# Kernel optimization log

Hardware: AMD Instinct MI355X
Metric: run time of the kernel (lower is better)

The kernel has to match this reference:

```python
import jax, jax.numpy as jnp
import numpy as np

L = 4          # encoder layers
D = 1280       # d_model
H = 20         # heads
DH = D // H
FF = 5120
MEL = 128
S = 1500       # post-conv seq len
EPS = 1e-6


def quant_per_token(x):
    # dynamic per-token int8 quant: scale = max|x|/127
    s = jnp.max(jnp.abs(x), axis=-1, keepdims=True) / 127.0
    s = jnp.maximum(s, 1e-8)
    q = jnp.clip(jnp.round(x / s), -128, 127)
    return q, s


def w8a8_linear(qx, sx, w, b):
    # per-output-channel int8 weight quant, W8A8 GEMM, fp dequant epilogue
    ws = jnp.maximum(jnp.max(jnp.abs(w), axis=1, keepdims=True) / 127.0, 1e-8)  # [O,1]
    qw = jnp.clip(jnp.round(w / ws), -128, 127)
    y = qx @ qw.T                        # int-valued accum in fp32
    return y * sx * ws[:, 0][None, :] + b[None, :]


def rmsnorm_quant(x, w, b):
    # rms_norm_general: w * x / sqrt(E[x^2]+eps) + b, then per-token quant
    inv = jax.lax.rsqrt(jnp.mean(x * x, axis=-1, keepdims=True) + EPS)
    return quant_per_token(x * inv * w[None, :] + b[None, :])


def conv1d(x, w, b, stride, pad):
    y = jax.lax.conv_general_dilated(x, w, (stride,), [(pad, pad)],
                                     dimension_numbers=('NCW', 'OIW', 'NCW'))
    return y + b[None, :, None]


def setup_inputs() -> dict:
    key = jax.random.key(0)
    ks = jax.random.split(key, 24)
    n = lambda k, sh, sc=0.02: jax.random.normal(k, sh, jnp.float32) * sc
    return {
        'input_features': jax.random.normal(ks[0], (1, MEL, 2 * S), jnp.float32),
        'conv1_w': n(ks[1], (D, MEL, 3)), 'conv1_b': n(ks[2], (D,)),
        'conv2_w': n(ks[3], (D, D, 3)), 'conv2_b': n(ks[4], (D,)),
        'pos_emb': n(ks[5], (S, D)),
        'ln1_w': jnp.ones((L, D)), 'ln1_b': n(ks[6], (L, D)),
        'qkv_w': n(ks[7], (L, 3 * D, D)), 'qkv_b': n(ks[8], (L, 3 * D)),
        'out_w': n(ks[9], (L, D, D)), 'out_b': n(ks[10], (L, D)),
        'ln2_w': jnp.ones((L, D)), 'ln2_b': n(ks[11], (L, D)),
        'fc1_w': n(ks[12], (L, FF, D)), 'fc1_b': n(ks[13], (L, FF)),
        'fc2_w': n(ks[14], (L, D, FF)), 'fc2_b': n(ks[15], (L, D)),
        'lnf_w': jnp.ones((D,)), 'lnf_b': n(ks[16], (D,)),
    }


def reference(input_features, conv1_w, conv1_b, conv2_w, conv2_b, pos_emb,
              ln1_w, ln1_b, qkv_w, qkv_b, out_w, out_b,
              ln2_w, ln2_b, fc1_w, fc1_b, fc2_w, fc2_b, lnf_w, lnf_b):
    B = input_features.shape[0]
    h = jax.nn.gelu(conv1d(input_features, conv1_w, conv1_b, 1, 1))
    h = jax.nn.gelu(conv1d(h, conv2_w, conv2_b, 2, 1))
    h = h.transpose(0, 2, 1) + pos_emb[None]          # [B,S,D]
    h = h.reshape(B * S, D)
    scale = DH ** -0.5
    for l in range(L):
        res = h
        qx, sx = rmsnorm_quant(h, ln1_w[l], ln1_b[l])
        qkv = w8a8_linear(qx, sx, qkv_w[l], qkv_b[l])  # [B*S, 3D]
        q, k, v = jnp.split(qkv.reshape(B, S, 3, H, DH), 3, axis=2)
        q, k, v = q[:, :, 0], k[:, :, 0], v[:, :, 0]   # [B,S,H,DH]
        scores = jnp.einsum('bqhd,bkhd->bhqk', q, k) * scale
        attn = jax.nn.softmax(scores, axis=-1)
        ao = jnp.einsum('bhqk,bkhd->bqhd', attn, v).reshape(B * S, D)
        qa, sa = quant_per_token(ao)
        h = res + w8a8_linear(qa, sa, out_w[l], out_b[l])
        res = h
        qx, sx = rmsnorm_quant(h, ln2_w[l], ln2_b[l])
        f1 = w8a8_linear(qx, sx, fc1_w[l], fc1_b[l])
        qm, sm = quant_per_token(jax.nn.gelu(f1))
        h = res + w8a8_linear(qm, sm, fc2_w[l], fc2_b[l])
    h = h.reshape(B, S, D)
    # avg_pooler: AvgPool1d(kernel=2, stride=2) over time
    h = h.reshape(B, S // 2, 2, D).mean(axis=2)
    # final LayerNorm (true layernorm, fp path)
    mu = jnp.mean(h, axis=-1, keepdims=True)
    var = jnp.mean(jnp.square(h - mu), axis=-1, keepdims=True)
    h = (h - mu) * jax.lax.rsqrt(var + 1e-5) * lnf_w + lnf_b
    return h
```

## Files before the change

### kernel.cpp

```cpp
#include <hip/hip_runtime.h>
#include <stdint.h>

#define S_LEN 1500
#define D_MODEL 1280
#define N_HEAD 20
#define D_HEAD 64
#define FF_DIM 5120
#define N_LAYER 4

typedef int v4i __attribute__((ext_vector_type(4)));


__device__ inline float gelu_tanh(float x) {
    float x3 = x * x * x;
    return 0.5f * x * (1.0f + tanhf(0.7978845608028654f * (x + 0.044715f * x3)));
}

__device__ inline float wred_sum(float v) {
    for (int o = 32; o > 0; o >>= 1) v += __shfl_down(v, o, 64);
    return v;
}
__device__ inline float wred_max(float v) {
    for (int o = 32; o > 0; o >>= 1) v = fmaxf(v, __shfl_down(v, o, 64));
    return v;
}
__device__ inline float block_sum(float v, float* sm4) {
    v = wred_sum(v);
    int w = threadIdx.x >> 6;
    if ((threadIdx.x & 63) == 0) sm4[w] = v;
    __syncthreads();
    float r = sm4[0] + sm4[1] + sm4[2] + sm4[3];
    __syncthreads();
    return r;
}
__device__ inline float block_max(float v, float* sm4) {
    v = wred_max(v);
    int w = threadIdx.x >> 6;
    if ((threadIdx.x & 63) == 0) sm4[w] = v;
    __syncthreads();
    float r = fmaxf(fmaxf(sm4[0], sm4[1]), fmaxf(sm4[2], sm4[3]));
    __syncthreads();
    return r;
}


__global__ __launch_bounds__(256) void im2col1_kernel(
    const float* __restrict__ x, float* __restrict__ A1)
{
    int t = blockIdx.x * 256 + threadIdx.x;
    int col = blockIdx.y;
    if (t >= 3000) return;
    int tap = col >> 7, i = col & 127;
    int src = t - 1 + tap;
    float v = (src >= 0 && src < 3000) ? x[(size_t)i * 3000 + src] : 0.0f;
    A1[(size_t)t * 384 + col] = v;
}

__global__ __launch_bounds__(256) void im2col2_kernel(
    const float* __restrict__ g1, float* __restrict__ A2)
{
    int col = blockIdx.x * 256 + threadIdx.x;
    int t = blockIdx.y;
    if (col >= 3840) return;
    int tap = col / 1280, o = col - tap * 1280;
    int src = 2 * t - 1 + tap;
    float v = (src >= 0 && src < 3000) ? g1[(size_t)src * 1280 + o] : 0.0f;
    A2[(size_t)t * 3840 + col] = v;
}

__global__ __launch_bounds__(256) void wreorder_kernel(
    const float* __restrict__ w, float* __restrict__ wo, int C)
{
    int o = blockIdx.x;
    int KC = 3 * C;
    const float* wr = w + (size_t)o * KC;
    float* orow = wo + (size_t)o * KC;
    for (int col = threadIdx.x; col < KC; col += 256) {
        int tap = col / C, i = col - tap * C;
        orow[col] = wr[i * 3 + tap];
    }
}

template <int EPI>
__global__ __launch_bounds__(256) void gemm_f32_kernel(
    const float* __restrict__ A, const float* __restrict__ W,
    const float* __restrict__ bias, const float* __restrict__ pos,
    float* __restrict__ out, int M, int N, int K)
{
    __shared__ float As[16][68];
    __shared__ float Bs[16][68];
    int tid = threadIdx.x;
    int tx = tid & 15, ty = tid >> 4;
    int m0 = blockIdx.y * 64, n0 = blockIdx.x * 64;
    int lr = tid >> 2;
    int lk = (tid & 3) * 4;
    int am = m0 + lr; if (am >= M) am = M - 1;
    const float* Ap = A + (size_t)am * K + lk;
    const float* Wp = W + (size_t)(n0 + lr) * K + lk;
    float c[4][4] = {};
    for (int k0 = 0; k0 < K; k0 += 16) {
        float4 av = *(const float4*)(Ap + k0);
        float4 wv = *(const float4*)(Wp + k0);
        __syncthreads();
        As[lk + 0][lr] = av.x; As[lk + 1][lr] = av.y; As[lk + 2][lr] = av.z; As[lk + 3][lr] = av.w;
        Bs[lk + 0][lr] = wv.x; Bs[lk + 1][lr] = wv.y; Bs[lk + 2][lr] = wv.z; Bs[lk + 3][lr] = wv.w;
        __syncthreads();
        #pragma unroll
        for (int kk = 0; kk < 16; kk++) {
            float4 a4 = *(const float4*)&As[kk][ty * 4];
            float4 b4 = *(const float4*)&Bs[kk][tx * 4];
            float ar[4] = {a4.x, a4.y, a4.z, a4.w};
            float br[4] = {b4.x, b4.y, b4.z, b4.w};
            #pragma unroll
            for (int i = 0; i < 4; i++)
                #pragma unroll
                for (int j = 0; j < 4; j++)
                    c[i][j] += ar[i] * br[j];
        }
    }
    #pragma unroll
    for (int i = 0; i < 4; i++) {
        int m = m0 + ty * 4 + i;
        if (m >= M) continue;
        #pragma unroll
        for (int j = 0; j < 4; j++) {
            int n = n0 + tx * 4 + j;
            float v = gelu_tanh(c[i][j] + bias[n]);
            if (EPI == 1) v += pos[(size_t)m * N + n];
            out[(size_t)m * N + n] = v;
        }
    }
}


__global__ __launch_bounds__(256) void wquant_kernel(
    const float* __restrict__ w, int8_t* __restrict__ qw,
    float* __restrict__ ws, int K)
{
    int r = blockIdx.x;
    int tid = threadIdx.x;
    __shared__ float sm4[4];
    const float4* wr = (const float4*)(w + (size_t)r * K);
    int n4 = K >> 2;
    float mx = 0.0f;
    for (int i = tid; i < n4; i += 256) {
        float4 v = wr[i];
        mx = fmaxf(mx, fmaxf(fmaxf(fabsf(v.x), fabsf(v.y)), fmaxf(fabsf(v.z), fabsf(v.w))));
    }
    mx = block_max(mx, sm4);
    float sc = fmaxf(mx / 127.0f, 1e-8f);
    if (tid == 0) ws[r] = sc;
    float rs = 1.0f / sc;
    char4* qr = (char4*)(qw + (size_t)r * K);
    for (int i = tid; i < n4; i += 256) {
        float4 v = wr[i];
        char4 q;
        q.x = (int8_t)fminf(fmaxf(rintf(v.x * rs), -128.0f), 127.0f);
        q.y = (int8_t)fminf(fmaxf(rintf(v.y * rs), -128.0f), 127.0f);
        q.z = (int8_t)fminf(fmaxf(rintf(v.z * rs), -128.0f), 127.0f);
        q.w = (int8_t)fminf(fmaxf(rintf(v.w * rs), -128.0f), 127.0f);
        qr[i] = q;
    }
}

__global__ __launch_bounds__(256) void rmsnorm_quant_kernel(
    const float* __restrict__ x, const float* __restrict__ w,
    const float* __restrict__ b, int8_t* __restrict__ q,
    float* __restrict__ sx)
{
    int s = blockIdx.x;
    int tid = threadIdx.x;
    __shared__ float sm4[4];
    const float* xr = x + (size_t)s * D_MODEL;
    float v[5];
    float ss = 0.0f;
    for (int i = 0; i < 5; i++) {
        float t = xr[tid + 256 * i];
        v[i] = t;
        ss += t * t;
    }
    ss = block_sum(ss, sm4);
    float inv = rsqrtf(ss * (1.0f / 1280.0f) + 1e-6f);
    float mx = 0.0f;
    for (int i = 0; i < 5; i++) {
        int idx = tid + 256 * i;
        float t = v[i] * inv * w[idx] + b[idx];
        v[i] = t;
        mx = fmaxf(mx, fabsf(t));
    }
    mx = block_max(mx, sm4);
    float sc = fmaxf(mx / 127.0f, 1e-8f);
    if (tid == 0) sx[s] = sc;
    float rs = 1.0f / sc;
    for (int i = 0; i < 5; i++) {
        float qv = rintf(v[i] * rs);
        qv = fminf(fmaxf(qv, -128.0f), 127.0f);
        q[(size_t)s * D_MODEL + tid + 256 * i] = (int8_t)qv;
    }
}

template <bool GELU>
__global__ __launch_bounds__(256) void quant_kernel(
    const float* __restrict__ x, int8_t* __restrict__ q,
    float* __restrict__ sx, int Dm)
{
    int s = blockIdx.x;
    int tid = threadIdx.x;
    __shared__ float sm4[4];
    const float4* xr = (const float4*)(x + (size_t)s * Dm);
    int n4 = Dm >> 2;
    float mx = 0.0f;
    for (int i = tid; i < n4; i += 256) {
        float4 t = xr[i];
        if (GELU) { t.x = gelu_tanh(t.x); t.y = gelu_tanh(t.y); t.z = gelu_tanh(t.z); t.w = gelu_tanh(t.w); }
        mx = fmaxf(mx, fmaxf(fmaxf(fabsf(t.x), fabsf(t.y)), fmaxf(fabsf(t.z), fabsf(t.w))));
    }
    mx = block_max(mx, sm4);
    float sc = fmaxf(mx / 127.0f, 1e-8f);
    if (tid == 0) sx[s] = sc;
    float rs = 1.0f / sc;
    char4* qr = (char4*)(q + (size_t)s * Dm);
    for (int i = tid; i < n4; i += 256) {
        float4 t = xr[i];
        if (GELU) { t.x = gelu_tanh(t.x); t.y = gelu_tanh(t.y); t.z = gelu_tanh(t.z); t.w = gelu_tanh(t.w); }
        char4 qq;
        qq.x = (int8_t)fminf(fmaxf(rintf(t.x * rs), -128.0f), 127.0f);
        qq.y = (int8_t)fminf(fmaxf(rintf(t.y * rs), -128.0f), 127.0f);
        qq.z = (int8_t)fminf(fmaxf(rintf(t.z * rs), -128.0f), 127.0f);
        qq.w = (int8_t)fminf(fmaxf(rintf(t.w * rs), -128.0f), 127.0f);
        qr[i] = qq;
    }
}

__global__ __launch_bounds__(256) void gemm_w8a8_mfma(
    const int8_t* __restrict__ qx, const float* __restrict__ sx,
    const int8_t* __restrict__ qw, const float* __restrict__ ws,
    const float* __restrict__ bias, const float* __restrict__ res,
    float* __restrict__ out, int M, int O, int K)
{
    int lane = threadIdx.x & 63;
    int wv = threadIdx.x >> 6;
    int l15 = lane & 15;
    int quad = lane >> 4;
    int m_base = blockIdx.y * 64 + wv * 16;
    int n_base = blockIdx.x * 64;

    int ar = m_base + l15; if (ar >= M) ar = M - 1;
    const int8_t* ap = qx + (size_t)ar * K + quad * 16;
    const int8_t* bp = qw + (size_t)(n_base + l15) * K + quad * 16;
    size_t rowK16 = (size_t)16 * K;

    v4i acc0 = {0, 0, 0, 0}, acc1 = {0, 0, 0, 0}, acc2 = {0, 0, 0, 0}, acc3 = {0, 0, 0, 0};
    int nsteps = K >> 6;
    for (int s = 0; s < nsteps; s++) {
        v4i a  = *(const v4i*)(ap + s * 64);
        v4i b0 = *(const v4i*)(bp + s * 64);
        v4i b1 = *(const v4i*)(bp + rowK16 + s * 64);
        v4i b2 = *(const v4i*)(bp + 2 * rowK16 + s * 64);
        v4i b3 = *(const v4i*)(bp + 3 * rowK16 + s * 64);
        acc0 = __builtin_amdgcn_mfma_i32_16x16x64_i8(a, b0, acc0, 0, 0, 0);
        acc1 = __builtin_amdgcn_mfma_i32_16x16x64_i8(a, b1, acc1, 0, 0, 0);
        acc2 = __builtin_amdgcn_mfma_i32_16x16x64_i8(a, b2, acc2, 0, 0, 0);
        acc3 = __builtin_amdgcn_mfma_i32_16x16x64_i8(a, b3, acc3, 0, 0, 0);
    }

    float sxv[4];
    #pragma unroll
    for (int r = 0; r < 4; r++) {
        int m = m_base + quad * 4 + r;
        sxv[r] = (m < M) ? sx[m] : 0.0f;
    }
    v4i accs[4] = {acc0, acc1, acc2, acc3};
    #pragma unroll
    for (int nb = 0; nb < 4; nb++) {
        int n = n_base + nb * 16 + l15;
        float wn = ws[n];
        float bn = bias[n];
        #pragma unroll
        for (int r = 0; r < 4; r++) {
            int m = m_base + quad * 4 + r;
            if (m < M) {
                float y = (float)accs[nb][r] * sxv[r] * wn + bn;
                if (res) y += res[(size_t)m * O + n];
                out[(size_t)m * O + n] = y;
            }
        }
    }
}

__global__ __launch_bounds__(256) void attn_tiled_kernel(
    const float* __restrict__ qkv, float* __restrict__ ao)
{
    __shared__ float Qs[64][68];
    __shared__ float KV[64][68];
    __shared__ float Ps[64][68];
    int h = blockIdx.y;
    int q_tile = blockIdx.x;
    int tid = threadIdx.x;
    int tx = tid & 15, ty = tid >> 4;
    int q0 = ty * 4;
    int d0 = tx * 4;

    {
        int r = tid >> 2;
        int dq = (tid & 3) * 16;
        int qg = q_tile * 64 + r;
        int qc = qg < S_LEN ? qg : S_LEN - 1;
        const float4* src = (const float4*)(qkv + (size_t)qc * 3840 + h * 64 + dq);
        #pragma unroll
        for (int i = 0; i < 4; i++)
            *(float4*)&Qs[r][dq + i * 4] = src[i];
    }

    float O[4][4] = {};
    float m_run[4], l_run[4];
    #pragma unroll
    for (int i = 0; i < 4; i++) { m_run[i] = -INFINITY; l_run[i] = 0.0f; }

    for (int kt = 0; kt < 24; kt++) {
        int kbase = kt * 64;
        int krem = S_LEN - kbase;

        __syncthreads();
        {
            int kk = tid >> 2;
            int dq = (tid & 3) * 16;
            int kg = kbase + kk;
            int kc = kg < S_LEN ? kg : S_LEN - 1;
            const float4* src = (const float4*)(qkv + (size_t)kc * 3840 + 1280 + h * 64 + dq);
            #pragma unroll
            for (int i = 0; i < 4; i++) {
                float4 v = src[i];
                KV[dq + i * 4 + 0][kk] = v.x;
                KV[dq + i * 4 + 1][kk] = v.y;
                KV[dq + i * 4 + 2][kk] = v.z;
                KV[dq + i * 4 + 3][kk] = v.w;
            }
        }
        __syncthreads();

        float s[4][4] = {};
        int k0loc = tx * 4;
        for (int d = 0; d < 64; d += 4) {
            float4 qv[4], kv[4];
            #pragma unroll
            for (int i = 0; i < 4; i++) qv[i] = *(const float4*)&Qs[q0 + i][d];
            #pragma unroll
            for (int dd = 0; dd < 4; dd++) kv[dd] = *(const float4*)&KV[d + dd][k0loc];
            #pragma unroll
            for (int i = 0; i < 4; i++) {
                float qa[4] = {qv[i].x, qv[i].y, qv[i].z, qv[i].w};
                #pragma unroll
                for (int dd = 0; dd < 4; dd++) {
                    float kb[4] = {kv[dd].x, kv[dd].y, kv[dd].z, kv[dd].w};
                    #pragma unroll
                    for (int j = 0; j < 4; j++)
                        s[i][j] += qa[dd] * kb[j];
                }
            }
        }

        #pragma unroll
        for (int i = 0; i < 4; i++)
            #pragma unroll
            for (int j = 0; j < 4; j++) {
                s[i][j] *= 0.125f;
                if (k0loc + j >= krem) s[i][j] = -INFINITY;
            }

        #pragma unroll
        for (int i = 0; i < 4; i++) {
            float t = fmaxf(fmaxf(s[i][0], s[i][1]), fmaxf(s[i][2], s[i][3]));
            #pragma unroll
            for (int msk = 1; msk < 16; msk <<= 1)
                t = fmaxf(t, __shfl_xor(t, msk, 64));
            float mn = fmaxf(m_run[i], t);
            float alpha = __expf(m_run[i] - mn);
            m_run[i] = mn;
            float rs = 0.0f;
            #pragma unroll
            for (int j = 0; j < 4; j++) {
                float p = __expf(s[i][j] - mn);
                s[i][j] = p;
                rs += p;
            }
            #pragma unroll
            for (int msk = 1; msk < 16; msk <<= 1)
                rs += __shfl_xor(rs, msk, 64);
            l_run[i] = l_run[i] * alpha + rs;
            #pragma unroll
            for (int j = 0; j < 4; j++) O[i][j] *= alpha;
            *(float4*)&Ps[q0 + i][k0loc] = *(float4*)&s[i][0];
        }
        __syncthreads();

        {
            int kk = tid >> 2;
            int dq = (tid & 3) * 16;
            int kg = kbase + kk;
            int kc = kg < S_LEN ? kg : S_LEN - 1;
            const float4* src = (const float4*)(qkv + (size_t)kc * 3840 + 2560 + h * 64 + dq);
            #pragma unroll
            for (int i = 0; i < 4; i++)
                *(float4*)&KV[kk][dq + i * 4] = src[i];
        }
        __syncthreads();

        for (int kb = 0; kb < 64; kb += 4) {
            float4 pv[4], vv[4];
            #pragma unroll
            for (int i = 0; i < 4; i++) pv[i] = *(const float4*)&Ps[q0 + i][kb];
            #pragma unroll
            for (int kk = 0; kk < 4; kk++) vv[kk] = *(const float4*)&KV[kb + kk][d0];
            #pragma unroll
            for (int i = 0; i < 4; i++) {
                float pa[4] = {pv[i].x, pv[i].y, pv[i].z, pv[i].w};
                #pragma unroll
                for (int kk = 0; kk < 4; kk++) {
                    float vb[4] = {vv[kk].x, vv[kk].y, vv[kk].z, vv[kk].w};
                    #pragma unroll
                    for (int j = 0; j < 4; j++)
                        O[i][j] += pa[kk] * vb[j];
                }
            }
        }
    }

    #pragma unroll
    for (int i = 0; i < 4; i++) {
        int qg = q_tile * 64 + q0 + i;
        if (qg < S_LEN) {
            float rl = 1.0f / l_run[i];
            float4 o;
            o.x = O[i][0] * rl; o.y = O[i][1] * rl; o.z = O[i][2] * rl; o.w = O[i][3] * rl;
            *(float4*)(ao + (size_t)qg * D_MODEL + h * 64 + d0) = o;
        }
    }
}

__global__ __launch_bounds__(256) void pool_ln_kernel(
    const float* __restrict__ h, const float* __restrict__ w,
    const float* __restrict__ b, float* __restrict__ out)
{
    int t = blockIdx.x;
    int tid = threadIdx.x;
    __shared__ float sm4[4];
    const float* r0 = h + (size_t)(2 * t) * D_MODEL;
    const float* r1 = r0 + D_MODEL;
    float v[5];
    float s1 = 0.0f;
    for (int i = 0; i < 5; i++) {
        int idx = tid + 256 * i;
        float x = 0.5f * (r0[idx] + r1[idx]);
        v[i] = x;
        s1 += x;
    }
    float mu = block_sum(s1, sm4) * (1.0f / 1280.0f);
    float s2 = 0.0f;
    for (int i = 0; i < 5; i++) {
        float d = v[i] - mu;
        s2 += d * d;
    }
    float var = block_sum(s2, sm4) * (1.0f / 1280.0f);
    float inv = rsqrtf(var + 1e-5f);
    for (int i = 0; i < 5; i++) {
        int idx = tid + 256 * i;
        out[(size_t)t * D_MODEL + idx] = (v[i] - mu) * inv * w[idx] + b[idx];
    }
}


static inline size_t al256(size_t x) { return (x + 255) & ~(size_t)255; }

extern "C" void kernel_launch(void* const* d_in, const int* in_sizes, int n_in,
                              void* d_out, int out_size, void* d_ws, size_t ws_size,
                              hipStream_t stream) {
    const float* in_feat = (const float*)d_in[0];
    const float* conv1_w = (const float*)d_in[1];
    const float* conv1_b = (const float*)d_in[2];
    const float* conv2_w = (const float*)d_in[3];
    const float* conv2_b = (const float*)d_in[4];
    const float* pos_emb = (const float*)d_in[5];
    const float* ln1_w   = (const float*)d_in[6];
    const float* ln1_b   = (const float*)d_in[7];
    const float* qkv_w   = (const float*)d_in[8];
    const float* qkv_b   = (const float*)d_in[9];
    const float* out_w   = (const float*)d_in[10];
    const float* out_b   = (const float*)d_in[11];
    const float* ln2_w   = (const float*)d_in[12];
    const float* ln2_b   = (const float*)d_in[13];
    const float* fc1_w   = (const float*)d_in[14];
    const float* fc1_b   = (const float*)d_in[15];
    const float* fc2_w   = (const float*)d_in[16];
    const float* fc2_b   = (const float*)d_in[17];
    const float* lnf_w   = (const float*)d_in[18];
    const float* lnf_b   = (const float*)d_in[19];
    float* outp = (float*)d_out;

    char* ws = (char*)d_ws;
    size_t off = 0;
    auto carve = [&](size_t bytes) {
        void* p = ws + off;
        off += al256(bytes);
        return p;
    };
    float*  hA      = (float*)carve((size_t)S_LEN * D_MODEL * 4);
    float*  hB      = (float*)carve((size_t)S_LEN * D_MODEL * 4);
    float*  qkvbuf  = (float*)carve((size_t)S_LEN * 3840 * 4);
    float*  aobuf   = (float*)carve((size_t)S_LEN * D_MODEL * 4);
    float*  f1buf   = (float*)carve((size_t)S_LEN * FF_DIM * 4);
    int8_t* q8      = (int8_t*)carve((size_t)S_LEN * FF_DIM);
    float*  sx      = (float*)carve((size_t)S_LEN * 4);
    int8_t* qw_qkv  = (int8_t*)carve((size_t)3840 * 1280);
    float*  ws_qkv  = (float*)carve((size_t)3840 * 4);
    int8_t* qw_out  = (int8_t*)carve((size_t)1280 * 1280);
    float*  ws_out  = (float*)carve((size_t)1280 * 4);
    int8_t* qw_fc1  = (int8_t*)carve((size_t)5120 * 1280);
    float*  ws_fc1  = (float*)carve((size_t)5120 * 4);
    int8_t* qw_fc2  = (int8_t*)carve((size_t)1280 * 5120);
    float*  ws_fc2  = (float*)carve((size_t)1280 * 4);
    (void)ws_size; (void)n_in; (void)in_sizes; (void)out_size;

    float* A1  = (float*)q8;
    float* W1r = aobuf;
    float* g1  = qkvbuf;
    float* A2  = f1buf;
    float* W2r = qkvbuf;

    im2col1_kernel<<<dim3(12, 384), 256, 0, stream>>>(in_feat, A1);
    wreorder_kernel<<<1280, 256, 0, stream>>>(conv1_w, W1r, 128);
    gemm_f32_kernel<0><<<dim3(20, 47), 256, 0, stream>>>(A1, W1r, conv1_b, nullptr, g1, 3000, 1280, 384);
    im2col2_kernel<<<dim3(15, 1500), 256, 0, stream>>>(g1, A2);
    wreorder_kernel<<<1280, 256, 0, stream>>>(conv2_w, W2r, 1280);
    gemm_f32_kernel<1><<<dim3(20, 24), 256, 0, stream>>>(A2, W2r, conv2_b, pos_emb, hA, 1500, 1280, 3840);

    float* h = hA;
    float* hn = hB;
    const int mtiles = (S_LEN + 63) / 64;

    for (int l = 0; l < N_LAYER; l++) {
        wquant_kernel<<<3840, 256, 0, stream>>>(qkv_w + (size_t)l * 3840 * 1280, qw_qkv, ws_qkv, 1280);
        wquant_kernel<<<1280, 256, 0, stream>>>(out_w + (size_t)l * 1280 * 1280, qw_out, ws_out, 1280);
        wquant_kernel<<<5120, 256, 0, stream>>>(fc1_w + (size_t)l * 5120 * 1280, qw_fc1, ws_fc1, 1280);
        wquant_kernel<<<1280, 256, 0, stream>>>(fc2_w + (size_t)l * 1280 * 5120, qw_fc2, ws_fc2, 5120);

        rmsnorm_quant_kernel<<<S_LEN, 256, 0, stream>>>(h, ln1_w + l * D_MODEL, ln1_b + l * D_MODEL, q8, sx);
        gemm_w8a8_mfma<<<dim3(60, mtiles), 256, 0, stream>>>(q8, sx, qw_qkv, ws_qkv,
            qkv_b + (size_t)l * 3840, nullptr, qkvbuf, S_LEN, 3840, 1280);
        attn_tiled_kernel<<<dim3(24, N_HEAD), 256, 0, stream>>>(qkvbuf, aobuf);
        quant_kernel<false><<<S_LEN, 256, 0, stream>>>(aobuf, q8, sx, D_MODEL);
        gemm_w8a8_mfma<<<dim3(20, mtiles), 256, 0, stream>>>(q8, sx, qw_out, ws_out,
            out_b + (size_t)l * 1280, h, hn, S_LEN, 1280, 1280);
        { float* t = h; h = hn; hn = t; }

        rmsnorm_quant_kernel<<<S_LEN, 256, 0, stream>>>(h, ln2_w + l * D_MODEL, ln2_b + l * D_MODEL, q8, sx);
        gemm_w8a8_mfma<<<dim3(80, mtiles), 256, 0, stream>>>(q8, sx, qw_fc1, ws_fc1,
            fc1_b + (size_t)l * 5120, nullptr, f1buf, S_LEN, 5120, 1280);
        quant_kernel<true><<<S_LEN, 256, 0, stream>>>(f1buf, q8, sx, FF_DIM);
        gemm_w8a8_mfma<<<dim3(20, mtiles), 256, 0, stream>>>(q8, sx, qw_fc2, ws_fc2,
            fc2_b + (size_t)l * 1280, h, hn, S_LEN, 1280, 5120);
        { float* t = h; h = hn; hn = t; }
    }

    pool_ln_kernel<<<750, 256, 0, stream>>>(h, lnf_w, lnf_b, outp);
}
```

Measured before the change: 2.740 ms.

## Run conv GEMMs on bf16x3 split-precision MFMA instead of scalar fp32

```diff
diff --git a/kernel.cpp b/kernel.cpp
--- a/kernel.cpp
+++ b/kernel.cpp
@@ -9,6 +9,8 @@
 #define N_LAYER 4
 
 typedef int v4i __attribute__((ext_vector_type(4)));
+typedef short v8s __attribute__((ext_vector_type(8)));
+typedef float v4f __attribute__((ext_vector_type(4)));
 
 
 __device__ inline float gelu_tanh(float x) {
@@ -43,9 +45,19 @@
     return r;
 }
 
+__device__ inline unsigned short f2bf(float x) {
+    unsigned int u = __float_as_uint(x);
+    u += 0x7fffu + ((u >> 16) & 1u);
+    return (unsigned short)(u >> 16);
+}
+__device__ inline float bf2f(unsigned short h) {
+    return __uint_as_float(((unsigned int)h) << 16);
+}
+
 
 __global__ __launch_bounds__(256) void im2col1_kernel(
-    const float* __restrict__ x, float* __restrict__ A1)
+    const float* __restrict__ x, unsigned short* __restrict__ Ah,
+    unsigned short* __restrict__ Al)
 {
     int t = blockIdx.x * 256 + threadIdx.x;
     int col = blockIdx.y;
@@ -53,11 +65,14 @@
     int tap = col >> 7, i = col & 127;
     int src = t - 1 + tap;
     float v = (src >= 0 && src < 3000) ? x[(size_t)i * 3000 + src] : 0.0f;
-    A1[(size_t)t * 384 + col] = v;
+    unsigned short h = f2bf(v);
+    Ah[(size_t)t * 384 + col] = h;
+    Al[(size_t)t * 384 + col] = f2bf(v - bf2f(h));
 }
 
 __global__ __launch_bounds__(256) void im2col2_kernel(
-    const float* __restrict__ g1, float* __restrict__ A2)
+    const float* __restrict__ g1, unsigned short* __restrict__ Ah,
+    unsigned short* __restrict__ Al)
 {
     int col = blockIdx.x * 256 + threadIdx.x;
     int t = blockIdx.y;
@@ -65,69 +80,78 @@
     int tap = col / 1280, o = col - tap * 1280;
     int src = 2 * t - 1 + tap;
     float v = (src >= 0 && src < 3000) ? g1[(size_t)src * 1280 + o] : 0.0f;
-    A2[(size_t)t * 3840 + col] = v;
+    unsigned short h = f2bf(v);
+    Ah[(size_t)t * 3840 + col] = h;
+    Al[(size_t)t * 3840 + col] = f2bf(v - bf2f(h));
 }
 
 __global__ __launch_bounds__(256) void wreorder_kernel(
-    const float* __restrict__ w, float* __restrict__ wo, int C)
+    const float* __restrict__ w, unsigned short* __restrict__ woh,
+    unsigned short* __restrict__ wol, int C)
 {
     int o = blockIdx.x;
     int KC = 3 * C;
     const float* wr = w + (size_t)o * KC;
-    float* orow = wo + (size_t)o * KC;
     for (int col = threadIdx.x; col < KC; col += 256) {
         int tap = col / C, i = col - tap * C;
-        orow[col] = wr[i * 3 + tap];
+        float v = wr[i * 3 + tap];
+        unsigned short h = f2bf(v);
+        woh[(size_t)o * KC + col] = h;
+        wol[(size_t)o * KC + col] = f2bf(v - bf2f(h));
     }
 }
 
 template <int EPI>
-__global__ __launch_bounds__(256) void gemm_f32_kernel(
-    const float* __restrict__ A, const float* __restrict__ W,
+__global__ __launch_bounds__(256) void gemm_bf16x3_kernel(
+    const unsigned short* __restrict__ Ah, const unsigned short* __restrict__ Al,
+    const unsigned short* __restrict__ Wh, const unsigned short* __restrict__ Wl,
     const float* __restrict__ bias, const float* __restrict__ pos,
     float* __restrict__ out, int M, int N, int K)
 {
-    __shared__ float As[16][68];
-    __shared__ float Bs[16][68];
-    int tid = threadIdx.x;
-    int tx = tid & 15, ty = tid >> 4;
-    int m0 = blockIdx.y * 64, n0 = blockIdx.x * 64;
-    int lr = tid >> 2;
-    int lk = (tid & 3) * 4;
-    int am = m0 + lr; if (am >= M) am = M - 1;
-    const float* Ap = A + (size_t)am * K + lk;
-    const float* Wp = W + (size_t)(n0 + lr) * K + lk;
-    float c[4][4] = {};
-    for (int k0 = 0; k0 < K; k0 += 16) {
-        float4 av = *(const float4*)(Ap + k0);
-        float4 wv = *(const float4*)(Wp + k0);
-        __syncthreads();
-        As[lk + 0][lr] = av.x; As[lk + 1][lr] = av.y; As[lk + 2][lr] = av.z; As[lk + 3][lr] = av.w;
-        Bs[lk + 0][lr] = wv.x; Bs[lk + 1][lr] = wv.y; Bs[lk + 2][lr] = wv.z; Bs[lk + 3][lr] = wv.w;
-        __syncthreads();
+    int lane = threadIdx.x & 63;
+    int wv = threadIdx.x >> 6;
+    int l15 = lane & 15;
+    int quad = lane >> 4;
+    int m_base = blockIdx.y * 64 + wv * 16;
+    int n_base = blockIdx.x * 64;
+
+    int ar = m_base + l15; if (ar >= M) ar = M - 1;
+    const unsigned short* aph = Ah + (size_t)ar * K + quad * 8;
+    const unsigned short* apl = Al + (size_t)ar * K + quad * 8;
+    const unsigned short* bph = Wh + (size_t)(n_base + l15) * K + quad * 8;
+    const unsigned short* bpl = Wl + (size_t)(n_base + l15) * K + quad * 8;
+    size_t rowK16 = (size_t)16 * K;
+
+    v4f acc[4];
+    #pragma unroll
+    for (int nb = 0; nb < 4; nb++) acc[nb] = (v4f){0.0f, 0.0f, 0.0f, 0.0f};
+
+    int nsteps = K >> 5;
+    for (int s = 0; s < nsteps; s++) {
+        v8s ah = *(const v8s*)(aph + s * 32);
+        v8s al = *(const v8s*)(apl + s * 32);
         #pragma unroll
-        for (int kk = 0; kk < 16; kk++) {
-            float4 a4 = *(const float4*)&As[kk][ty * 4];
-            float4 b4 = *(const float4*)&Bs[kk][tx * 4];
-            float ar[4] = {a4.x, a4.y, a4.z, a4.w};
-            float br[4] = {b4.x, b4.y, b4.z, b4.w};
-            #pragma unroll
-            for (int i = 0; i < 4; i++)
-                #pragma unroll
-                for (int j = 0; j < 4; j++)
-                    c[i][j] += ar[i] * br[j];
-        }
-    }
+        for (int nb = 0; nb < 4; nb++) {
+            v8s bh = *(const v8s*)(bph + (size_t)nb * rowK16 + s * 32);
+            v8s bl = *(const v8s*)(bpl + (size_t)nb * rowK16 + s * 32);
+            acc[nb] = __builtin_amdgcn_mfma_f32_16x16x32_bf16(ah, bh, acc[nb], 0, 0, 0);
+            acc[nb] = __builtin_amdgcn_mfma_f32_16x16x32_bf16(al, bh, acc[nb], 0, 0, 0);
+            acc[nb] = __builtin_amdgcn_mfma_f32_16x16x32_bf16(ah, bl, acc[nb], 0, 0, 0);
+        }
+    }
+
     #pragma unroll
-    for (int i = 0; i < 4; i++) {
-        int m = m0 + ty * 4 + i;
-        if (m >= M) continue;
+    for (int nb = 0; nb < 4; nb++) {
+        int n = n_base + nb * 16 + l15;
+        float bn = bias[n];
         #pragma unroll
-        for (int j = 0; j < 4; j++) {
-            int n = n0 + tx * 4 + j;
-            float v = gelu_tanh(c[i][j] + bias[n]);
-            if (EPI == 1) v += pos[(size_t)m * N + n];
-            out[(size_t)m * N + n] = v;
+        for (int r = 0; r < 4; r++) {
+            int m = m_base + quad * 4 + r;
+            if (m < M) {
+                float v = gelu_tanh(acc[nb][r] + bn);
+                if (EPI == 1) v += pos[(size_t)m * N + n];
+                out[(size_t)m * N + n] = v;
+            }
         }
     }
 }
@@ -521,18 +545,22 @@
     float*  ws_fc2  = (float*)carve((size_t)1280 * 4);
     (void)ws_size; (void)n_in; (void)in_sizes; (void)out_size;
 
-    float* A1  = (float*)q8;
-    float* W1r = aobuf;
-    float* g1  = qkvbuf;
-    float* A2  = f1buf;
-    float* W2r = qkvbuf;
-
-    im2col1_kernel<<<dim3(12, 384), 256, 0, stream>>>(in_feat, A1);
-    wreorder_kernel<<<1280, 256, 0, stream>>>(conv1_w, W1r, 128);
-    gemm_f32_kernel<0><<<dim3(20, 47), 256, 0, stream>>>(A1, W1r, conv1_b, nullptr, g1, 3000, 1280, 384);
-    im2col2_kernel<<<dim3(15, 1500), 256, 0, stream>>>(g1, A2);
-    wreorder_kernel<<<1280, 256, 0, stream>>>(conv2_w, W2r, 1280);
-    gemm_f32_kernel<1><<<dim3(20, 24), 256, 0, stream>>>(A2, W2r, conv2_b, pos_emb, hA, 1500, 1280, 3840);
+    unsigned short* A1h = (unsigned short*)q8;
+    unsigned short* A1l = A1h + (size_t)3000 * 384;
+    unsigned short* W1h = (unsigned short*)aobuf;
+    unsigned short* W1l = W1h + (size_t)1280 * 384;
+    float* g1 = qkvbuf;
+    unsigned short* A2h = (unsigned short*)f1buf;
+    unsigned short* A2l = A2h + (size_t)1500 * 3840;
+    unsigned short* W2h = (unsigned short*)qkvbuf;
+    unsigned short* W2l = W2h + (size_t)1280 * 3840;
+
+    im2col1_kernel<<<dim3(12, 384), 256, 0, stream>>>(in_feat, A1h, A1l);
+    wreorder_kernel<<<1280, 256, 0, stream>>>(conv1_w, W1h, W1l, 128);
+    gemm_bf16x3_kernel<0><<<dim3(20, 47), 256, 0, stream>>>(A1h, A1l, W1h, W1l, conv1_b, nullptr, g1, 3000, 1280, 384);
+    im2col2_kernel<<<dim3(15, 1500), 256, 0, stream>>>(g1, A2h, A2l);
+    wreorder_kernel<<<1280, 256, 0, stream>>>(conv2_w, W2h, W2l, 1280);
+    gemm_bf16x3_kernel<1><<<dim3(20, 24), 256, 0, stream>>>(A2h, A2l, W2h, W2l, conv2_b, pos_emb, hA, 1500, 1280, 3840);
 
     float* h = hA;
     float* hn = hB;
```

Measured after the change: 2.809 ms. 1.03x slower.
